# Performance work log

Measured on AMD Instinct MI355X. Metric: run time of the kernel, lower is better.

The kernel has to match this reference:

```python
import jax, jax.numpy as jnp
import numpy as np

B, S, NB, D, H = 4, 512, 32, 512, 8

def setup_inputs() -> dict:
    key = jax.random.key(0)
    ks = jax.random.split(key, 8)
    sc = 1.0 / np.sqrt(D)
    return {
        "query": jax.random.normal(ks[0], (B, S, NB, D), dtype=jnp.float32),
        "key": jax.random.normal(ks[1], (B, S, NB, D), dtype=jnp.float32),
        "value": jax.random.normal(ks[2], (B, S, NB, D), dtype=jnp.float32),
        "padding_mask": jnp.zeros((B, S, NB), dtype=jnp.float32),
        "wq": jax.random.normal(ks[3], (D, D), dtype=jnp.float32) * sc,
        "bq": jnp.zeros((D,), dtype=jnp.float32),
        "wk": jax.random.normal(ks[4], (D, D), dtype=jnp.float32) * sc,
        "bk": jnp.zeros((D,), dtype=jnp.float32),
        "wv": jax.random.normal(ks[5], (D, D), dtype=jnp.float32) * sc,
        "bv": jnp.zeros((D,), dtype=jnp.float32),
        "nhead": H,
    }

def reference(query, key, value, padding_mask, wq, bq, wk, bk, wv, bv, nhead):
    b, s, nb, d = query.shape
    dh = d // nhead
    # Linear projections (torch Linear: x @ W.T + b)
    Q = query @ wq.T + bq
    K = key @ wk.T + bk
    V = value @ wv.T + bv
    # [B, S, Nb, H, dh] -> [B, H, S, Nb, dh]
    def split_heads(x):
        return x.reshape(b, s, nb, nhead, dh).transpose(0, 3, 1, 2, 4)
    Qh, Kh, Vh = split_heads(Q), split_heads(K), split_heads(V)
    # attention over the block axis per (batch, head, seq position)
    logits = jnp.einsum('bhsnd,bhsmd->bhsnm', Qh, Kh) / jnp.sqrt(jnp.float32(dh))
    # additive mask [B, S, Nb] -> [B, 1, S, 1, Nb]
    logits = logits + padding_mask[:, None, :, None, :]
    attn_weight = jax.nn.softmax(logits, axis=-1)  # [B,H,S,Nb,Nb]
    attn_output = jnp.einsum('bhsnm,bhsmd->bhsnd', attn_weight, Vh)
    # [B,H,S,Nb,dh] -> [B,S,Nb,H,dh] -> [B,S,Nb,D]
    attn_output = attn_output.transpose(0, 2, 3, 1, 4).reshape(b, s, nb, d)
    return (attn_output, attn_weight)
```

## Files before the change

kernel.cpp:

```cpp
#include <hip/hip_runtime.h>
#include <hip/hip_bf16.h>


#define NBD (32 * 512)
#define XS_STRIDE 516

typedef __bf16 bf16x8 __attribute__((ext_vector_type(8)));
typedef float f32x16 __attribute__((ext_vector_type(16)));

__device__ __forceinline__ unsigned f2b(float f) {
  union { float f; unsigned u; } v;
  v.f = f;
  return (v.u + 0x7fffu + ((v.u >> 16) & 1u)) >> 16;
}

__device__ __forceinline__ f32x16 mfma32(uint4 a, uint4 b, f32x16 c) {
  union { uint4 u; bf16x8 v; } ua, ub;
  ua.u = a;
  ub.u = b;
  return __builtin_amdgcn_mfma_f32_32x32x16_bf16(ua.v, ub.v, c, 0, 0, 0);
}

__device__ __forceinline__ uint4 ld_lds_64x2(const unsigned short* p, unsigned byteoff) {
  const char* c = (const char*)p;
  uint2 lo = *(const uint2*)(c + byteoff);
  uint2 hi = *(const uint2*)(c + byteoff + 8);
  uint4 r;
  r.x = lo.x; r.y = lo.y; r.z = hi.x; r.w = hi.y;
  return r;
}

__device__ __forceinline__ uint4 frag_cd(const unsigned* CP, int qb, int half) {
  const unsigned s0 = __shfl_xor(CP[qb + 0], 32);
  const unsigned s1 = __shfl_xor(CP[qb + 1], 32);
  const unsigned s2 = __shfl_xor(CP[qb + 2], 32);
  const unsigned s3 = __shfl_xor(CP[qb + 3], 32);
  uint4 f;
  f.x = half ? s2 : CP[qb + 0];
  f.y = half ? s3 : CP[qb + 1];
  f.z = half ? CP[qb + 2] : s0;
  f.w = half ? CP[qb + 3] : s1;
  return f;
}

__global__ void wconv_kernel(const float* __restrict__ wq,
                             const float* __restrict__ wk,
                             const float* __restrict__ wv,
                             uint4* __restrict__ out) {
  const int g = blockIdx.x * blockDim.x + threadIdx.x;
  const int m = g >> 15;
  const int j = g & 32767;
  const int l31 = j & 31;
  const int half = (j >> 5) & 1;
  const int k = (j >> 6) & 31;
  const int tile = j >> 11;
  const float* src = (m == 0) ? wq : (m == 1) ? wk : wv;
  const float4* p = (const float4*)(src + (size_t)(tile * 32 + l31) * 512 + k * 16 + half * 8);
  float4 f0 = p[0], f1 = p[1];
  uint4 o;
  o.x = f2b(f0.x) | (f2b(f0.y) << 16);
  o.y = f2b(f0.z) | (f2b(f0.w) << 16);
  o.z = f2b(f1.x) | (f2b(f1.y) << 16);
  o.w = f2b(f1.z) | (f2b(f1.w) << 16);
  out[g] = o;
}

__global__ __launch_bounds__(512, 4)
void mhba_kernel(const float* __restrict__ q_in, const float* __restrict__ k_in,
                 const float* __restrict__ v_in, const float* __restrict__ mask,
                 const float* __restrict__ bq, const float* __restrict__ bk,
                 const float* __restrict__ bv,
                 const uint4* __restrict__ wpk,
                 float* __restrict__ out_attn,
                 float* __restrict__ out_w) {
  __shared__ unsigned short Xs[32 * XS_STRIDE];
  __shared__ __align__(16) char SCR[8][4352];

  const int bs = blockIdx.x;
  const int tid = threadIdx.x;
  const int lane = tid & 63;
  const int h = tid >> 6;
  const int l31 = lane & 31;
  const int half = lane >> 5;

  const float* srcG[3] = {k_in, q_in, v_in};
  char* scr = &SCR[h][0];

  unsigned QT[2][8], VP[2][8];

#pragma unroll
  for (int m = 0; m < 3; ++m) {
    __syncthreads();
    const float4* src4 = (const float4*)(srcG[m] + (size_t)bs * NBD);
#pragma unroll
    for (int i = 0; i < 8; ++i) {
      const int idx4 = i * 512 + tid;
      float4 f = src4[idx4];
      const int n = idx4 >> 7;
      const int k4 = idx4 & 127;
      uint2 u;
      u.x = f2b(f.x) | (f2b(f.y) << 16);
      u.y = f2b(f.z) | (f2b(f.w) << 16);
      *(uint2*)((char*)Xs + (n * (XS_STRIDE * 2) + k4 * 8)) = u;
    }
    __syncthreads();

    const int wsel = (m == 0) ? 1 : (m == 1) ? 0 : 2;
    const uint4* w0 = wpk + wsel * 32768 + (2 * h) * 2048 + half * 32 + l31;
    const uint4* w1 = w0 + 2048;
    const unsigned abase = (unsigned)(l31 * (XS_STRIDE * 2) + half * 16);

    f32x16 acc0, acc1;
#pragma unroll
    for (int r = 0; r < 16; ++r) { acc0[r] = 0.0f; acc1[r] = 0.0f; }
#pragma unroll 8
    for (int k = 0; k < 32; ++k) {
      uint4 a = ld_lds_64x2(Xs, abase + (unsigned)k * 32);
      uint4 b0 = w0[k * 64];
      uint4 b1 = w1[k * 64];
      if (m == 1) {
        acc0 = mfma32(b0, a, acc0);
        acc1 = mfma32(b1, a, acc1);
      } else {
        acc0 = mfma32(a, b0, acc0);
        acc1 = mfma32(a, b1, acc1);
      }
    }

    if (m == 0) {
      const float bc0 = bk[h * 64 + l31];
      const float bc1 = bk[h * 64 + 32 + l31];
#pragma unroll
      for (int r = 0; r < 16; ++r) {
        const int n = (r & 3) + 8 * (r >> 2) + 4 * half;
        const unsigned base = (unsigned)(n * 128);
        const unsigned sw = (unsigned)(n & 7) << 4;
        *(unsigned short*)(scr + ((base + l31 * 2) ^ sw)) =
            (unsigned short)f2b(acc0[r] + bc0);
        *(unsigned short*)(scr + ((base + 64 + l31 * 2) ^ sw)) =
            (unsigned short)f2b(acc1[r] + bc1);
      }
    } else if (m == 1) {
#pragma unroll
      for (int q = 0; q < 8; ++q) {
        const int n0 = ((2 * q) & 3) + 8 * (q >> 1) + 4 * half;
        float2 bv0 = *(const float2*)(bq + h * 64 + n0);
        float2 bv1 = *(const float2*)(bq + h * 64 + 32 + n0);
        QT[0][q] = f2b(acc0[2 * q] + bv0.x) | (f2b(acc0[2 * q + 1] + bv0.y) << 16);
        QT[1][q] = f2b(acc1[2 * q] + bv1.x) | (f2b(acc1[2 * q + 1] + bv1.y) << 16);
      }
    } else {
      const float bc0 = bv[h * 64 + l31];
      const float bc1 = bv[h * 64 + 32 + l31];
#pragma unroll
      for (int q = 0; q < 8; ++q) {
        VP[0][q] = f2b(acc0[2 * q] + bc0) | (f2b(acc0[2 * q + 1] + bc0) << 16);
        VP[1][q] = f2b(acc1[2 * q] + bc1) | (f2b(acc1[2 * q + 1] + bc1) << 16);
      }
    }
  }

  f32x16 lg;
#pragma unroll
  for (int r = 0; r < 16; ++r) lg[r] = 0.0f;
#pragma unroll
  for (int kk = 0; kk < 4; ++kk) {
    const unsigned off =
        (unsigned)(l31 * 128 + kk * 32 + half * 16) ^ ((unsigned)(l31 & 7) << 4);
    uint4 ka = *(const uint4*)(scr + off);
    uint4 qf = frag_cd(QT[kk >> 1], (kk & 1) * 4, half);
    lg = mfma32(ka, qf, lg);
  }

  const float* mrow = mask + (size_t)bs * 32;
  float w[16];
#pragma unroll
  for (int q = 0; q < 8; ++q) {
    const int mm0 = ((2 * q) & 3) + 8 * (q >> 1) + 4 * half;
    float2 mk = *(const float2*)(mrow + mm0);
    w[2 * q] = lg[2 * q] * 0.125f + mk.x;
    w[2 * q + 1] = lg[2 * q + 1] * 0.125f + mk.y;
  }
  float mx = w[0];
#pragma unroll
  for (int r = 1; r < 16; ++r) mx = fmaxf(mx, w[r]);
  mx = fmaxf(mx, __shfl_xor(mx, 32));
  float ss = 0.0f;
#pragma unroll
  for (int r = 0; r < 16; ++r) {
    w[r] = __expf(w[r] - mx);
    ss += w[r];
  }
  ss += __shfl_xor(ss, 32);
  const float inv = __frcp_rn(ss);
#pragma unroll
  for (int r = 0; r < 16; ++r) w[r] *= inv;

  unsigned PP[8];
#pragma unroll
  for (int q = 0; q < 8; ++q)
    PP[q] = f2b(w[2 * q]) | (f2b(w[2 * q + 1]) << 16);

  float* scrF = (float*)scr;
#pragma unroll
  for (int r = 0; r < 16; ++r) {
    const int mm = (r & 3) + 8 * (r >> 2) + 4 * half;
    scrF[l31 * 33 + mm] = w[r];
  }
  const int b = bs >> 9;
  const int s = bs & 511;
  float* wout = out_w + ((size_t)((b * 8 + h) * 512 + s)) * 1024;
#pragma unroll
  for (int j = 0; j < 16; ++j) {
    const int n = 2 * j + half;
    wout[n * 32 + l31] = scrF[n * 33 + l31];
  }

  f32x16 o0, o1;
#pragma unroll
  for (int r = 0; r < 16; ++r) { o0[r] = 0.0f; o1[r] = 0.0f; }
#pragma unroll
  for (int kk = 0; kk < 2; ++kk) {
    uint4 pa = frag_cd(PP, 4 * kk, half);
    uint4 vb0 = frag_cd(VP[0], 4 * kk, half);
    uint4 vb1 = frag_cd(VP[1], 4 * kk, half);
    o0 = mfma32(pa, vb0, o0);
    o1 = mfma32(pa, vb1, o1);
  }

  float* obase = out_attn + (size_t)bs * NBD + h * 64 + l31;
#pragma unroll
  for (int r = 0; r < 16; ++r) {
    const int n = (r & 3) + 8 * (r >> 2) + 4 * half;
    obase[n * 512] = o0[r];
    obase[n * 512 + 32] = o1[r];
  }
}

extern "C" void kernel_launch(void* const* d_in, const int* in_sizes, int n_in,
                              void* d_out, int out_size, void* d_ws, size_t ws_size,
                              hipStream_t stream) {
  const float* q    = (const float*)d_in[0];
  const float* k    = (const float*)d_in[1];
  const float* v    = (const float*)d_in[2];
  const float* mask = (const float*)d_in[3];
  const float* wq   = (const float*)d_in[4];
  const float* bq   = (const float*)d_in[5];
  const float* wk   = (const float*)d_in[6];
  const float* bk   = (const float*)d_in[7];
  const float* wv   = (const float*)d_in[8];
  const float* bv   = (const float*)d_in[9];

  uint4* wpk = (uint4*)d_ws;
  float* out_attn = (float*)d_out;
  float* out_w = out_attn + (size_t)4 * 512 * 32 * 512;

  wconv_kernel<<<384, 256, 0, stream>>>(wq, wk, wv, wpk);
  mhba_kernel<<<2048, 512, 0, stream>>>(q, k, v, mask, bq, bk, bv, wpk,
                                        out_attn, out_w);
}
```

Before: 234.8 us.

## Process two sequence positions per block to reuse weight fragments

```diff
diff --git a/kernel.cpp b/kernel.cpp
--- a/kernel.cpp
+++ b/kernel.cpp
@@ -4,6 +4,7 @@
 
 #define NBD (32 * 512)
 #define XS_STRIDE 516
+#define XS_BYTES (32 * XS_STRIDE * 2)
 
 typedef __bf16 bf16x8 __attribute__((ext_vector_type(8)));
 typedef float f32x16 __attribute__((ext_vector_type(16)));
@@ -73,10 +74,9 @@
                  const uint4* __restrict__ wpk,
                  float* __restrict__ out_attn,
                  float* __restrict__ out_w) {
-  __shared__ unsigned short Xs[32 * XS_STRIDE];
-  __shared__ __align__(16) char SCR[8][4352];
-
-  const int bs = blockIdx.x;
+  __shared__ unsigned short Xs[2 * 32 * XS_STRIDE];
+
+  const int bs0 = blockIdx.x * 2;
   const int tid = threadIdx.x;
   const int lane = tid & 63;
   const int h = tid >> 6;
@@ -84,156 +84,187 @@
   const int half = lane >> 5;
 
   const float* srcG[3] = {k_in, q_in, v_in};
-  char* scr = &SCR[h][0];
-
-  unsigned QT[2][8], VP[2][8];
+
+  unsigned KT[2][2][8], QT[2][2][8], VPk[2][2][8];
+
+  const unsigned abase = (unsigned)(l31 * (XS_STRIDE * 2) + half * 16);
 
 #pragma unroll
   for (int m = 0; m < 3; ++m) {
     __syncthreads();
-    const float4* src4 = (const float4*)(srcG[m] + (size_t)bs * NBD);
-#pragma unroll
-    for (int i = 0; i < 8; ++i) {
-      const int idx4 = i * 512 + tid;
-      float4 f = src4[idx4];
-      const int n = idx4 >> 7;
-      const int k4 = idx4 & 127;
-      uint2 u;
-      u.x = f2b(f.x) | (f2b(f.y) << 16);
-      u.y = f2b(f.z) | (f2b(f.w) << 16);
-      *(uint2*)((char*)Xs + (n * (XS_STRIDE * 2) + k4 * 8)) = u;
+#pragma unroll
+    for (int j = 0; j < 2; ++j) {
+      const float4* s4 = (const float4*)(srcG[m] + (size_t)(bs0 + j) * NBD);
+#pragma unroll
+      for (int i = 0; i < 8; ++i) {
+        const int idx4 = i * 512 + tid;
+        float4 f = s4[idx4];
+        const int n = idx4 >> 7;
+        const int k4 = idx4 & 127;
+        uint2 u;
+        u.x = f2b(f.x) | (f2b(f.y) << 16);
+        u.y = f2b(f.z) | (f2b(f.w) << 16);
+        *(uint2*)((char*)Xs + (j * XS_BYTES + n * (XS_STRIDE * 2) + k4 * 8)) = u;
+      }
     }
     __syncthreads();
 
     const int wsel = (m == 0) ? 1 : (m == 1) ? 0 : 2;
-    const uint4* w0 = wpk + wsel * 32768 + (2 * h) * 2048 + half * 32 + l31;
-    const uint4* w1 = w0 + 2048;
-    const unsigned abase = (unsigned)(l31 * (XS_STRIDE * 2) + half * 16);
-
-    f32x16 acc0, acc1;
-#pragma unroll
-    for (int r = 0; r < 16; ++r) { acc0[r] = 0.0f; acc1[r] = 0.0f; }
+#pragma unroll
+    for (int t = 0; t < 2; ++t) {
+      const uint4* wld = wpk + wsel * 32768 + (2 * h + t) * 2048 + half * 32 + l31;
+      f32x16 acc0, acc1;
+#pragma unroll
+      for (int r = 0; r < 16; ++r) { acc0[r] = 0.0f; acc1[r] = 0.0f; }
 #pragma unroll 8
-    for (int k = 0; k < 32; ++k) {
-      uint4 a = ld_lds_64x2(Xs, abase + (unsigned)k * 32);
-      uint4 b0 = w0[k * 64];
-      uint4 b1 = w1[k * 64];
-      if (m == 1) {
-        acc0 = mfma32(b0, a, acc0);
-        acc1 = mfma32(b1, a, acc1);
+      for (int k = 0; k < 32; ++k) {
+        uint4 b = wld[k * 64];
+        uint4 a0 = ld_lds_64x2(Xs, abase + (unsigned)k * 32);
+        uint4 a1 = ld_lds_64x2(Xs, XS_BYTES + abase + (unsigned)k * 32);
+        if (m <= 1) {
+          acc0 = mfma32(b, a0, acc0);
+          acc1 = mfma32(b, a1, acc1);
+        } else {
+          acc0 = mfma32(a0, b, acc0);
+          acc1 = mfma32(a1, b, acc1);
+        }
+      }
+      if (m == 0) {
+#pragma unroll
+        for (int q = 0; q < 8; ++q) {
+          const int n0 = ((2 * q) & 3) + 8 * (q >> 1) + 4 * half;
+          float2 bb = *(const float2*)(bk + h * 64 + t * 32 + n0);
+          KT[0][t][q] = f2b(acc0[2 * q] + bb.x) | (f2b(acc0[2 * q + 1] + bb.y) << 16);
+          KT[1][t][q] = f2b(acc1[2 * q] + bb.x) | (f2b(acc1[2 * q + 1] + bb.y) << 16);
+        }
+      } else if (m == 1) {
+#pragma unroll
+        for (int q = 0; q < 8; ++q) {
+          const int n0 = ((2 * q) & 3) + 8 * (q >> 1) + 4 * half;
+          float2 bb = *(const float2*)(bq + h * 64 + t * 32 + n0);
+          QT[0][t][q] = f2b(acc0[2 * q] + bb.x) | (f2b(acc0[2 * q + 1] + bb.y) << 16);
+          QT[1][t][q] = f2b(acc1[2 * q] + bb.x) | (f2b(acc1[2 * q + 1] + bb.y) << 16);
+        }
       } else {
-        acc0 = mfma32(a, b0, acc0);
-        acc1 = mfma32(a, b1, acc1);
-      }
-    }
-
-    if (m == 0) {
-      const float bc0 = bk[h * 64 + l31];
-      const float bc1 = bk[h * 64 + 32 + l31];
-#pragma unroll
-      for (int r = 0; r < 16; ++r) {
-        const int n = (r & 3) + 8 * (r >> 2) + 4 * half;
-        const unsigned base = (unsigned)(n * 128);
-        const unsigned sw = (unsigned)(n & 7) << 4;
-        *(unsigned short*)(scr + ((base + l31 * 2) ^ sw)) =
-            (unsigned short)f2b(acc0[r] + bc0);
-        *(unsigned short*)(scr + ((base + 64 + l31 * 2) ^ sw)) =
-            (unsigned short)f2b(acc1[r] + bc1);
-      }
-    } else if (m == 1) {
+        const float bc = bv[h * 64 + t * 32 + l31];
+#pragma unroll
+        for (int q = 0; q < 8; ++q) {
+          VPk[0][t][q] = f2b(acc0[2 * q] + bc) | (f2b(acc0[2 * q + 1] + bc) << 16);
+          VPk[1][t][q] = f2b(acc1[2 * q] + bc) | (f2b(acc1[2 * q + 1] + bc) << 16);
+        }
+      }
+    }
+  }
+
+  __syncthreads();
+#pragma unroll
+  for (int j = 0; j < 2; ++j) {
+    char* vb = (char*)Xs + h * 8192 + j * 4096;
+#pragma unroll
+    for (int t = 0; t < 2; ++t)
 #pragma unroll
       for (int q = 0; q < 8; ++q) {
         const int n0 = ((2 * q) & 3) + 8 * (q >> 1) + 4 * half;
-        float2 bv0 = *(const float2*)(bq + h * 64 + n0);
-        float2 bv1 = *(const float2*)(bq + h * 64 + 32 + n0);
-        QT[0][q] = f2b(acc0[2 * q] + bv0.x) | (f2b(acc0[2 * q + 1] + bv0.y) << 16);
-        QT[1][q] = f2b(acc1[2 * q] + bv1.x) | (f2b(acc1[2 * q + 1] + bv1.y) << 16);
-      }
-    } else {
-      const float bc0 = bv[h * 64 + l31];
-      const float bc1 = bv[h * 64 + 32 + l31];
-#pragma unroll
-      for (int q = 0; q < 8; ++q) {
-        VP[0][q] = f2b(acc0[2 * q] + bc0) | (f2b(acc0[2 * q + 1] + bc0) << 16);
-        VP[1][q] = f2b(acc1[2 * q] + bc1) | (f2b(acc1[2 * q + 1] + bc1) << 16);
-      }
-    }
+        const unsigned col = (unsigned)((t * 32 + l31) * 2);
+        const unsigned pv = VPk[j][t][q];
+        *(unsigned short*)(vb + ((n0 * 128 + col) ^ ((unsigned)(n0 & 7) << 4))) =
+            (unsigned short)(pv & 0xffff);
+        *(unsigned short*)(vb + (((n0 + 1) * 128 + col) ^ ((unsigned)((n0 + 1) & 7) << 4))) =
+            (unsigned short)(pv >> 16);
+      }
   }
 
-  f32x16 lg;
-#pragma unroll
-  for (int r = 0; r < 16; ++r) lg[r] = 0.0f;
-#pragma unroll
-  for (int kk = 0; kk < 4; ++kk) {
-    const unsigned off =
-        (unsigned)(l31 * 128 + kk * 32 + half * 16) ^ ((unsigned)(l31 & 7) << 4);
-    uint4 ka = *(const uint4*)(scr + off);
-    uint4 qf = frag_cd(QT[kk >> 1], (kk & 1) * 4, half);
-    lg = mfma32(ka, qf, lg);
-  }
-
-  const float* mrow = mask + (size_t)bs * 32;
-  float w[16];
-#pragma unroll
-  for (int q = 0; q < 8; ++q) {
-    const int mm0 = ((2 * q) & 3) + 8 * (q >> 1) + 4 * half;
-    float2 mk = *(const float2*)(mrow + mm0);
-    w[2 * q] = lg[2 * q] * 0.125f + mk.x;
-    w[2 * q + 1] = lg[2 * q + 1] * 0.125f + mk.y;
-  }
-  float mx = w[0];
-#pragma unroll
-  for (int r = 1; r < 16; ++r) mx = fmaxf(mx, w[r]);
-  mx = fmaxf(mx, __shfl_xor(mx, 32));
-  float ss = 0.0f;
-#pragma unroll
-  for (int r = 0; r < 16; ++r) {
-    w[r] = __expf(w[r] - mx);
-    ss += w[r];
-  }
-  ss += __shfl_xor(ss, 32);
-  const float inv = __frcp_rn(ss);
-#pragma unroll
-  for (int r = 0; r < 16; ++r) w[r] *= inv;
-
-  unsigned PP[8];
-#pragma unroll
-  for (int q = 0; q < 8; ++q)
-    PP[q] = f2b(w[2 * q]) | (f2b(w[2 * q + 1]) << 16);
-
-  float* scrF = (float*)scr;
-#pragma unroll
-  for (int r = 0; r < 16; ++r) {
-    const int mm = (r & 3) + 8 * (r >> 2) + 4 * half;
-    scrF[l31 * 33 + mm] = w[r];
-  }
-  const int b = bs >> 9;
-  const int s = bs & 511;
-  float* wout = out_w + ((size_t)((b * 8 + h) * 512 + s)) * 1024;
-#pragma unroll
-  for (int j = 0; j < 16; ++j) {
-    const int n = 2 * j + half;
-    wout[n * 32 + l31] = scrF[n * 33 + l31];
-  }
-
-  f32x16 o0, o1;
-#pragma unroll
-  for (int r = 0; r < 16; ++r) { o0[r] = 0.0f; o1[r] = 0.0f; }
-#pragma unroll
-  for (int kk = 0; kk < 2; ++kk) {
-    uint4 pa = frag_cd(PP, 4 * kk, half);
-    uint4 vb0 = frag_cd(VP[0], 4 * kk, half);
-    uint4 vb1 = frag_cd(VP[1], 4 * kk, half);
-    o0 = mfma32(pa, vb0, o0);
-    o1 = mfma32(pa, vb1, o1);
-  }
-
-  float* obase = out_attn + (size_t)bs * NBD + h * 64 + l31;
-#pragma unroll
-  for (int r = 0; r < 16; ++r) {
-    const int n = (r & 3) + 8 * (r >> 2) + 4 * half;
-    obase[n * 512] = o0[r];
-    obase[n * 512 + 32] = o1[r];
+#pragma unroll
+  for (int j = 0; j < 2; ++j) {
+    const int bsj = bs0 + j;
+
+    f32x16 lg;
+#pragma unroll
+    for (int r = 0; r < 16; ++r) lg[r] = 0.0f;
+#pragma unroll
+    for (int kk = 0; kk < 4; ++kk) {
+      uint4 ka = frag_cd(KT[j][kk >> 1], (kk & 1) * 4, half);
+      uint4 qf = frag_cd(QT[j][kk >> 1], (kk & 1) * 4, half);
+      lg = mfma32(ka, qf, lg);
+    }
+
+    const float* mrow = mask + (size_t)bsj * 32;
+    float w[16];
+#pragma unroll
+    for (int q = 0; q < 8; ++q) {
+      const int mm0 = ((2 * q) & 3) + 8 * (q >> 1) + 4 * half;
+      float2 mk = *(const float2*)(mrow + mm0);
+      w[2 * q] = lg[2 * q] * 0.125f + mk.x;
+      w[2 * q + 1] = lg[2 * q + 1] * 0.125f + mk.y;
+    }
+    float mx = w[0];
+#pragma unroll
+    for (int r = 1; r < 16; ++r) mx = fmaxf(mx, w[r]);
+    mx = fmaxf(mx, __shfl_xor(mx, 32));
+    float ss = 0.0f;
+#pragma unroll
+    for (int r = 0; r < 16; ++r) {
+      w[r] = __expf(w[r] - mx);
+      ss += w[r];
+    }
+    ss += __shfl_xor(ss, 32);
+    const float inv = __frcp_rn(ss);
+#pragma unroll
+    for (int r = 0; r < 16; ++r) w[r] *= inv;
+
+    unsigned PP[8];
+#pragma unroll
+    for (int q = 0; q < 8; ++q)
+      PP[q] = f2b(w[2 * q]) | (f2b(w[2 * q + 1]) << 16);
+
+    const char* vb = (const char*)Xs + h * 8192 + j * 4096;
+    f32x16 o0, o1;
+#pragma unroll
+    for (int r = 0; r < 16; ++r) { o0[r] = 0.0f; o1[r] = 0.0f; }
+#pragma unroll
+    for (int kk = 0; kk < 2; ++kk) {
+      uint4 pa = frag_cd(PP, 4 * kk, half);
+      unsigned pk0[4] = {0, 0, 0, 0}, pk1[4] = {0, 0, 0, 0};
+#pragma unroll
+      for (int jj = 0; jj < 8; ++jj) {
+        const int mr = kk * 16 + half * 8 + jj;
+        const unsigned sw = (unsigned)(mr & 7) << 4;
+        const unsigned v0 = *(const unsigned short*)(vb + ((mr * 128 + l31 * 2) ^ sw));
+        const unsigned v1 = *(const unsigned short*)(vb + ((mr * 128 + 64 + l31 * 2) ^ sw));
+        pk0[jj >> 1] |= v0 << ((jj & 1) * 16);
+        pk1[jj >> 1] |= v1 << ((jj & 1) * 16);
+      }
+      uint4 b0, b1;
+      b0.x = pk0[0]; b0.y = pk0[1]; b0.z = pk0[2]; b0.w = pk0[3];
+      b1.x = pk1[0]; b1.y = pk1[1]; b1.z = pk1[2]; b1.w = pk1[3];
+      o0 = mfma32(pa, b0, o0);
+      o1 = mfma32(pa, b1, o1);
+    }
+
+    asm volatile("" ::: "memory");
+    char* sc = (char*)Xs + h * 8192 + j * 4096;
+#pragma unroll
+    for (int r = 0; r < 16; ++r) {
+      const int mm = (r & 3) + 8 * (r >> 2) + 4 * half;
+      *(float*)(sc + ((l31 * 128 + mm * 4) ^ ((unsigned)(l31 & 7) << 4))) = w[r];
+    }
+    const int b = bsj >> 9;
+    const int s = bsj & 511;
+    float* wout = out_w + ((size_t)((b * 8 + h) * 512 + s)) * 1024;
+#pragma unroll
+    for (int jj = 0; jj < 16; ++jj) {
+      const int n = 2 * jj + half;
+      wout[n * 32 + l31] =
+          *(const float*)(sc + ((n * 128 + l31 * 4) ^ ((unsigned)(n & 7) << 4)));
+    }
+
+    float* obase = out_attn + (size_t)bsj * NBD + h * 64 + l31;
+#pragma unroll
+    for (int r = 0; r < 16; ++r) {
+      const int n = (r & 3) + 8 * (r >> 2) + 4 * half;
+      obase[n * 512] = o0[r];
+      obase[n * 512 + 32] = o1[r];
+    }
   }
 }
 
@@ -256,6 +287,6 @@
   float* out_w = out_attn + (size_t)4 * 512 * 32 * 512;
 
   wconv_kernel<<<384, 256, 0, stream>>>(wq, wk, wv, wpk);
-  mhba_kernel<<<2048, 512, 0, stream>>>(q, k, v, mask, bq, bk, bv, wpk,
+  mhba_kernel<<<1024, 512, 0, stream>>>(q, k, v, mask, bq, bk, bv, wpk,
                                         out_attn, out_w);
 }
```

New measurement: 630.4 us. +168.5%, slower.

## Process two positions per block with double-buffered LDS and prefetched global loads

Applied to the files above, without the earlier changes.

```diff
diff --git a/kernel.cpp b/kernel.cpp
--- a/kernel.cpp
+++ b/kernel.cpp
@@ -4,6 +4,7 @@
 
 #define NBD (32 * 512)
 #define XS_STRIDE 516
+#define XS_BYTES (32 * XS_STRIDE * 2)
 
 typedef __bf16 bf16x8 __attribute__((ext_vector_type(8)));
 typedef float f32x16 __attribute__((ext_vector_type(16)));
@@ -65,7 +66,7 @@
   out[g] = o;
 }
 
-__global__ __launch_bounds__(512, 4)
+__global__ __launch_bounds__(512, 2)
 void mhba_kernel(const float* __restrict__ q_in, const float* __restrict__ k_in,
                  const float* __restrict__ v_in, const float* __restrict__ mask,
                  const float* __restrict__ bq, const float* __restrict__ bk,
@@ -73,168 +74,182 @@
                  const uint4* __restrict__ wpk,
                  float* __restrict__ out_attn,
                  float* __restrict__ out_w) {
-  __shared__ unsigned short Xs[32 * XS_STRIDE];
-  __shared__ __align__(16) char SCR[8][4352];
-
-  const int bs = blockIdx.x;
+  __shared__ unsigned short Xs[2 * 2 * 32 * XS_STRIDE];
+
+  const int bs0 = blockIdx.x * 2;
   const int tid = threadIdx.x;
   const int lane = tid & 63;
   const int h = tid >> 6;
   const int l31 = lane & 31;
   const int half = lane >> 5;
 
-  const float* srcG[3] = {k_in, q_in, v_in};
-  char* scr = &SCR[h][0];
-
-  unsigned QT[2][8], VP[2][8];
-
-#pragma unroll
-  for (int m = 0; m < 3; ++m) {
-    __syncthreads();
-    const float4* src4 = (const float4*)(srcG[m] + (size_t)bs * NBD);
-#pragma unroll
-    for (int i = 0; i < 8; ++i) {
-      const int idx4 = i * 512 + tid;
-      float4 f = src4[idx4];
-      const int n = idx4 >> 7;
-      const int k4 = idx4 & 127;
-      uint2 u;
-      u.x = f2b(f.x) | (f2b(f.y) << 16);
-      u.y = f2b(f.z) | (f2b(f.w) << 16);
-      *(uint2*)((char*)Xs + (n * (XS_STRIDE * 2) + k4 * 8)) = u;
-    }
-    __syncthreads();
-
-    const int wsel = (m == 0) ? 1 : (m == 1) ? 0 : 2;
-    const uint4* w0 = wpk + wsel * 32768 + (2 * h) * 2048 + half * 32 + l31;
-    const uint4* w1 = w0 + 2048;
-    const unsigned abase = (unsigned)(l31 * (XS_STRIDE * 2) + half * 16);
-
-    f32x16 acc0, acc1;
-#pragma unroll
-    for (int r = 0; r < 16; ++r) { acc0[r] = 0.0f; acc1[r] = 0.0f; }
-#pragma unroll 8
-    for (int k = 0; k < 32; ++k) {
-      uint4 a = ld_lds_64x2(Xs, abase + (unsigned)k * 32);
-      uint4 b0 = w0[k * 64];
-      uint4 b1 = w1[k * 64];
-      if (m == 1) {
-        acc0 = mfma32(b0, a, acc0);
-        acc1 = mfma32(b1, a, acc1);
-      } else {
-        acc0 = mfma32(a, b0, acc0);
-        acc1 = mfma32(a, b1, acc1);
-      }
-    }
-
-    if (m == 0) {
-      const float bc0 = bk[h * 64 + l31];
-      const float bc1 = bk[h * 64 + 32 + l31];
-#pragma unroll
-      for (int r = 0; r < 16; ++r) {
-        const int n = (r & 3) + 8 * (r >> 2) + 4 * half;
-        const unsigned base = (unsigned)(n * 128);
-        const unsigned sw = (unsigned)(n & 7) << 4;
-        *(unsigned short*)(scr + ((base + l31 * 2) ^ sw)) =
-            (unsigned short)f2b(acc0[r] + bc0);
-        *(unsigned short*)(scr + ((base + 64 + l31 * 2) ^ sw)) =
-            (unsigned short)f2b(acc1[r] + bc1);
-      }
-    } else if (m == 1) {
-#pragma unroll
-      for (int q = 0; q < 8; ++q) {
-        const int n0 = ((2 * q) & 3) + 8 * (q >> 1) + 4 * half;
-        float2 bv0 = *(const float2*)(bq + h * 64 + n0);
-        float2 bv1 = *(const float2*)(bq + h * 64 + 32 + n0);
-        QT[0][q] = f2b(acc0[2 * q] + bv0.x) | (f2b(acc0[2 * q + 1] + bv0.y) << 16);
-        QT[1][q] = f2b(acc1[2 * q] + bv1.x) | (f2b(acc1[2 * q + 1] + bv1.y) << 16);
-      }
-    } else {
-      const float bc0 = bv[h * 64 + l31];
-      const float bc1 = bv[h * 64 + 32 + l31];
-#pragma unroll
-      for (int q = 0; q < 8; ++q) {
-        VP[0][q] = f2b(acc0[2 * q] + bc0) | (f2b(acc0[2 * q + 1] + bc0) << 16);
-        VP[1][q] = f2b(acc1[2 * q] + bc1) | (f2b(acc1[2 * q + 1] + bc1) << 16);
-      }
-    }
-  }
-
-  f32x16 lg;
-#pragma unroll
-  for (int r = 0; r < 16; ++r) lg[r] = 0.0f;
-#pragma unroll
-  for (int kk = 0; kk < 4; ++kk) {
-    const unsigned off =
-        (unsigned)(l31 * 128 + kk * 32 + half * 16) ^ ((unsigned)(l31 & 7) << 4);
-    uint4 ka = *(const uint4*)(scr + off);
-    uint4 qf = frag_cd(QT[kk >> 1], (kk & 1) * 4, half);
-    lg = mfma32(ka, qf, lg);
-  }
-
-  const float* mrow = mask + (size_t)bs * 32;
-  float w[16];
-#pragma unroll
-  for (int q = 0; q < 8; ++q) {
-    const int mm0 = ((2 * q) & 3) + 8 * (q >> 1) + 4 * half;
-    float2 mk = *(const float2*)(mrow + mm0);
-    w[2 * q] = lg[2 * q] * 0.125f + mk.x;
-    w[2 * q + 1] = lg[2 * q + 1] * 0.125f + mk.y;
-  }
-  float mx = w[0];
-#pragma unroll
-  for (int r = 1; r < 16; ++r) mx = fmaxf(mx, w[r]);
-  mx = fmaxf(mx, __shfl_xor(mx, 32));
-  float ss = 0.0f;
-#pragma unroll
-  for (int r = 0; r < 16; ++r) {
-    w[r] = __expf(w[r] - mx);
-    ss += w[r];
-  }
-  ss += __shfl_xor(ss, 32);
-  const float inv = __frcp_rn(ss);
-#pragma unroll
-  for (int r = 0; r < 16; ++r) w[r] *= inv;
-
-  unsigned PP[8];
-#pragma unroll
-  for (int q = 0; q < 8; ++q)
-    PP[q] = f2b(w[2 * q]) | (f2b(w[2 * q + 1]) << 16);
-
-  float* scrF = (float*)scr;
-#pragma unroll
-  for (int r = 0; r < 16; ++r) {
-    const int mm = (r & 3) + 8 * (r >> 2) + 4 * half;
-    scrF[l31 * 33 + mm] = w[r];
-  }
-  const int b = bs >> 9;
-  const int s = bs & 511;
-  float* wout = out_w + ((size_t)((b * 8 + h) * 512 + s)) * 1024;
-#pragma unroll
-  for (int j = 0; j < 16; ++j) {
-    const int n = 2 * j + half;
-    wout[n * 32 + l31] = scrF[n * 33 + l31];
-  }
-
-  f32x16 o0, o1;
-#pragma unroll
-  for (int r = 0; r < 16; ++r) { o0[r] = 0.0f; o1[r] = 0.0f; }
-#pragma unroll
-  for (int kk = 0; kk < 2; ++kk) {
-    uint4 pa = frag_cd(PP, 4 * kk, half);
-    uint4 vb0 = frag_cd(VP[0], 4 * kk, half);
-    uint4 vb1 = frag_cd(VP[1], 4 * kk, half);
-    o0 = mfma32(pa, vb0, o0);
-    o1 = mfma32(pa, vb1, o1);
-  }
-
-  float* obase = out_attn + (size_t)bs * NBD + h * 64 + l31;
-#pragma unroll
-  for (int r = 0; r < 16; ++r) {
-    const int n = (r & 3) + 8 * (r >> 2) + 4 * half;
-    obase[n * 512] = o0[r];
-    obase[n * 512 + 32] = o1[r];
-  }
+  unsigned short* bufA = Xs;
+  unsigned short* bufB = Xs + 2 * 32 * XS_STRIDE;
+
+  unsigned KT[2][2][8], QT[2][2][8], VP[2][2][8];
+  const unsigned abase = (unsigned)(l31 * (XS_STRIDE * 2) + half * 16);
+
+  float4 st[16];
+
+#define LOADS(SRC)                                                        \
+  {                                                                       \
+    _Pragma("unroll") for (int j = 0; j < 2; ++j) {                       \
+      const float4* s4 = (const float4*)((SRC) + (size_t)(bs0 + j) * NBD);\
+      _Pragma("unroll") for (int i = 0; i < 8; ++i)                       \
+        st[j * 8 + i] = s4[i * 512 + tid];                                \
+    }                                                                     \
+  }
+
+#define WRITE(BUF)                                                        \
+  {                                                                       \
+    _Pragma("unroll") for (int j = 0; j < 2; ++j) {                       \
+      _Pragma("unroll") for (int i = 0; i < 8; ++i) {                     \
+        const int idx4 = i * 512 + tid;                                   \
+        const int n = idx4 >> 7;                                          \
+        const int k4 = idx4 & 127;                                        \
+        float4 f = st[j * 8 + i];                                         \
+        uint2 u;                                                          \
+        u.x = f2b(f.x) | (f2b(f.y) << 16);                                \
+        u.y = f2b(f.z) | (f2b(f.w) << 16);                                \
+        *(uint2*)((char*)(BUF) + (j * XS_BYTES + n * (XS_STRIDE * 2) + k4 * 8)) = u; \
+      }                                                                   \
+    }                                                                     \
+  }
+
+#define COMPUTE(MM, BUF, WSEL, BIAS, DST, TRANSPOSED)                     \
+  {                                                                       \
+    _Pragma("unroll") for (int t = 0; t < 2; ++t) {                       \
+      const uint4* wld = wpk + (WSEL)*32768 + (2 * h + t) * 2048 + half * 32 + l31; \
+      f32x16 acc0, acc1;                                                  \
+      _Pragma("unroll") for (int r = 0; r < 16; ++r) { acc0[r] = 0.0f; acc1[r] = 0.0f; } \
+      _Pragma("unroll 8") for (int k = 0; k < 32; ++k) {                  \
+        uint4 b = wld[k * 64];                                            \
+        uint4 a0 = ld_lds_64x2((BUF), abase + (unsigned)k * 32);          \
+        uint4 a1 = ld_lds_64x2((BUF), XS_BYTES + abase + (unsigned)k * 32);\
+        if (TRANSPOSED) {                                                 \
+          acc0 = mfma32(b, a0, acc0);                                     \
+          acc1 = mfma32(b, a1, acc1);                                     \
+        } else {                                                          \
+          acc0 = mfma32(a0, b, acc0);                                     \
+          acc1 = mfma32(a1, b, acc1);                                     \
+        }                                                                 \
+      }                                                                   \
+      if (TRANSPOSED) {                                                   \
+        _Pragma("unroll") for (int q = 0; q < 8; ++q) {                   \
+          const int n0 = ((2 * q) & 3) + 8 * (q >> 1) + 4 * half;         \
+          float2 bb = *(const float2*)((BIAS) + h * 64 + t * 32 + n0);    \
+          DST[0][t][q] = f2b(acc0[2 * q] + bb.x) | (f2b(acc0[2 * q + 1] + bb.y) << 16); \
+          DST[1][t][q] = f2b(acc1[2 * q] + bb.x) | (f2b(acc1[2 * q + 1] + bb.y) << 16); \
+        }                                                                 \
+      } else {                                                            \
+        const float bc = (BIAS)[h * 64 + t * 32 + l31];                   \
+        _Pragma("unroll") for (int q = 0; q < 8; ++q) {                   \
+          DST[0][t][q] = f2b(acc0[2 * q] + bc) | (f2b(acc0[2 * q + 1] + bc) << 16); \
+          DST[1][t][q] = f2b(acc1[2 * q] + bc) | (f2b(acc1[2 * q + 1] + bc) << 16); \
+        }                                                                 \
+      }                                                                   \
+    }                                                                     \
+  }
+
+  LOADS(k_in);
+  WRITE(bufA);
+  __syncthreads();
+
+  LOADS(q_in);
+  COMPUTE(0, bufA, 1, bk, KT, 1);
+  WRITE(bufB);
+  __syncthreads();
+
+  LOADS(v_in);
+  COMPUTE(1, bufB, 0, bq, QT, 1);
+  WRITE(bufA);
+  __syncthreads();
+
+  COMPUTE(2, bufA, 2, bv, VP, 0);
+
+  asm volatile("" ::: "memory");
+  float* scrF = (float*)((char*)bufB + h * 8256);
+
+#pragma unroll
+  for (int j = 0; j < 2; ++j) {
+    const int bsj = bs0 + j;
+
+    f32x16 lg;
+#pragma unroll
+    for (int r = 0; r < 16; ++r) lg[r] = 0.0f;
+#pragma unroll
+    for (int kk = 0; kk < 4; ++kk) {
+      uint4 ka = frag_cd(KT[j][kk >> 1], (kk & 1) * 4, half);
+      uint4 qf = frag_cd(QT[j][kk >> 1], (kk & 1) * 4, half);
+      lg = mfma32(ka, qf, lg);
+    }
+
+    const float* mrow = mask + (size_t)bsj * 32;
+    float w[16];
+#pragma unroll
+    for (int q = 0; q < 8; ++q) {
+      const int mm0 = ((2 * q) & 3) + 8 * (q >> 1) + 4 * half;
+      float2 mk = *(const float2*)(mrow + mm0);
+      w[2 * q] = lg[2 * q] * 0.125f + mk.x;
+      w[2 * q + 1] = lg[2 * q + 1] * 0.125f + mk.y;
+    }
+    float mx = w[0];
+#pragma unroll
+    for (int r = 1; r < 16; ++r) mx = fmaxf(mx, w[r]);
+    mx = fmaxf(mx, __shfl_xor(mx, 32));
+    float ss = 0.0f;
+#pragma unroll
+    for (int r = 0; r < 16; ++r) {
+      w[r] = __expf(w[r] - mx);
+      ss += w[r];
+    }
+    ss += __shfl_xor(ss, 32);
+    const float inv = __frcp_rn(ss);
+#pragma unroll
+    for (int r = 0; r < 16; ++r) w[r] *= inv;
+
+    unsigned PP[8];
+#pragma unroll
+    for (int q = 0; q < 8; ++q)
+      PP[q] = f2b(w[2 * q]) | (f2b(w[2 * q + 1]) << 16);
+
+#pragma unroll
+    for (int r = 0; r < 16; ++r) {
+      const int mm = (r & 3) + 8 * (r >> 2) + 4 * half;
+      scrF[l31 * 33 + mm] = w[r];
+    }
+    const int b = bsj >> 9;
+    const int s = bsj & 511;
+    float* wout = out_w + ((size_t)((b * 8 + h) * 512 + s)) * 1024;
+#pragma unroll
+    for (int jj = 0; jj < 16; ++jj) {
+      const int n = 2 * jj + half;
+      wout[n * 32 + l31] = scrF[n * 33 + l31];
+    }
+
+    f32x16 o0, o1;
+#pragma unroll
+    for (int r = 0; r < 16; ++r) { o0[r] = 0.0f; o1[r] = 0.0f; }
+#pragma unroll
+    for (int kk = 0; kk < 2; ++kk) {
+      uint4 pa = frag_cd(PP, 4 * kk, half);
+      uint4 vb0 = frag_cd(VP[j][0], 4 * kk, half);
+      uint4 vb1 = frag_cd(VP[j][1], 4 * kk, half);
+      o0 = mfma32(pa, vb0, o0);
+      o1 = mfma32(pa, vb1, o1);
+    }
+
+    float* obase = out_attn + (size_t)bsj * NBD + h * 64 + l31;
+#pragma unroll
+    for (int r = 0; r < 16; ++r) {
+      const int n = (r & 3) + 8 * (r >> 2) + 4 * half;
+      obase[n * 512] = o0[r];
+      obase[n * 512 + 32] = o1[r];
+    }
+  }
+#undef LOADS
+#undef WRITE
+#undef COMPUTE
 }
 
 extern "C" void kernel_launch(void* const* d_in, const int* in_sizes, int n_in,
@@ -256,6 +271,6 @@
   float* out_w = out_attn + (size_t)4 * 512 * 32 * 512;
 
   wconv_kernel<<<384, 256, 0, stream>>>(wq, wk, wv, wpk);
-  mhba_kernel<<<2048, 512, 0, stream>>>(q, k, v, mask, bq, bk, bv, wpk,
+  mhba_kernel<<<1024, 512, 0, stream>>>(q, k, v, mask, bq, bk, bv, wpk,
                                         out_attn, out_w);
 }
```

After: 350.3 us. 49.2% more time.

## Double-buffer half-tile input staging to overlap global loads with MFMA

Applied to the files above, without the earlier changes.

```diff
diff --git a/kernel.cpp b/kernel.cpp
--- a/kernel.cpp
+++ b/kernel.cpp
@@ -3,7 +3,8 @@
 
 
 #define NBD (32 * 512)
-#define XS_STRIDE 516
+#define XH_STRIDE 260
+#define XH_BYTES (32 * XH_STRIDE * 2)
 
 typedef __bf16 bf16x8 __attribute__((ext_vector_type(8)));
 typedef float f32x16 __attribute__((ext_vector_type(16)));
@@ -73,7 +74,7 @@
                  const uint4* __restrict__ wpk,
                  float* __restrict__ out_attn,
                  float* __restrict__ out_w) {
-  __shared__ unsigned short Xs[32 * XS_STRIDE];
+  __shared__ unsigned short Xs[2][32 * XH_STRIDE];
   __shared__ __align__(16) char SCR[8][4352];
 
   const int bs = blockIdx.x;
@@ -83,93 +84,141 @@
   const int l31 = lane & 31;
   const int half = lane >> 5;
 
-  const float* srcG[3] = {k_in, q_in, v_in};
   char* scr = &SCR[h][0];
+  const float* srcs[3] = {k_in, q_in, v_in};
 
   unsigned QT[2][8], VP[2][8];
-
-#pragma unroll
-  for (int m = 0; m < 3; ++m) {
-    __syncthreads();
-    const float4* src4 = (const float4*)(srcG[m] + (size_t)bs * NBD);
-#pragma unroll
-    for (int i = 0; i < 8; ++i) {
-      const int idx4 = i * 512 + tid;
-      float4 f = src4[idx4];
-      const int n = idx4 >> 7;
-      const int k4 = idx4 & 127;
-      uint2 u;
-      u.x = f2b(f.x) | (f2b(f.y) << 16);
-      u.y = f2b(f.z) | (f2b(f.w) << 16);
-      *(uint2*)((char*)Xs + (n * (XS_STRIDE * 2) + k4 * 8)) = u;
+  const unsigned abase = (unsigned)(l31 * (XH_STRIDE * 2) + half * 16);
+
+  float4 st[4];
+
+#define STAGE_LOAD(M, H1)                                                  \
+  {                                                                        \
+    const float4* s4 = (const float4*)(srcs[M] + (size_t)bs * NBD);        \
+    _Pragma("unroll") for (int i = 0; i < 4; ++i) {                        \
+      const int idx4 = i * 512 + tid;                                      \
+      st[i] = s4[(idx4 >> 6) * 128 + (H1)*64 + (idx4 & 63)];               \
+    }                                                                      \
+  }
+
+#define STAGE_WRITE(P)                                                     \
+  {                                                                        \
+    _Pragma("unroll") for (int i = 0; i < 4; ++i) {                        \
+      const int idx4 = i * 512 + tid;                                      \
+      const int n = idx4 >> 6, k4 = idx4 & 63;                             \
+      uint2 u;                                                             \
+      u.x = f2b(st[i].x) | (f2b(st[i].y) << 16);                           \
+      u.y = f2b(st[i].z) | (f2b(st[i].w) << 16);                           \
+      *(uint2*)((char*)Xs[P] + (n * (XH_STRIDE * 2) + k4 * 8)) = u;        \
+    }                                                                      \
+  }
+
+#define COMPUTE_HALF(P, WSEL, H1, TRANSPOSED)                              \
+  {                                                                        \
+    const uint4* w0 = wpk + (WSEL)*32768 + (2 * h) * 2048 + (H1)*1024 +    \
+                      half * 32 + l31;                                     \
+    const uint4* w1 = w0 + 2048;                                           \
+    _Pragma("unroll 8") for (int k = 0; k < 16; ++k) {                     \
+      uint4 a = ld_lds_64x2(Xs[P], abase + (unsigned)k * 32);              \
+      uint4 b0 = w0[k * 64];                                               \
+      uint4 b1 = w1[k * 64];                                               \
+      if (TRANSPOSED) {                                                    \
+        acc0 = mfma32(b0, a, acc0);                                        \
+        acc1 = mfma32(b1, a, acc1);                                        \
+      } else {                                                             \
+        acc0 = mfma32(a, b0, acc0);                                        \
+        acc1 = mfma32(a, b1, acc1);                                        \
+      }                                                                    \
+    }                                                                      \
+  }
+
+  f32x16 acc0, acc1;
+#pragma unroll
+  for (int r = 0; r < 16; ++r) { acc0[r] = 0.0f; acc1[r] = 0.0f; }
+
+  STAGE_LOAD(0, 0);
+  STAGE_WRITE(0);
+  __syncthreads();
+
+  STAGE_LOAD(0, 1);
+  COMPUTE_HALF(0, 1, 0, 0);
+  STAGE_WRITE(1);
+  __syncthreads();
+
+  STAGE_LOAD(1, 0);
+  COMPUTE_HALF(1, 1, 1, 0);
+  {
+    const float bc0 = bk[h * 64 + l31];
+    const float bc1 = bk[h * 64 + 32 + l31];
+#pragma unroll
+    for (int r = 0; r < 16; ++r) {
+      const int n = (r & 3) + 8 * (r >> 2) + 4 * half;
+      const unsigned base = (unsigned)(n * 128);
+      const unsigned sw = (unsigned)(n & 7) << 4;
+      *(unsigned short*)(scr + ((base + l31 * 2) ^ sw)) =
+          (unsigned short)f2b(acc0[r] + bc0);
+      *(unsigned short*)(scr + ((base + 64 + l31 * 2) ^ sw)) =
+          (unsigned short)f2b(acc1[r] + bc1);
+      acc0[r] = 0.0f;
+      acc1[r] = 0.0f;
     }
-    __syncthreads();
-
-    const int wsel = (m == 0) ? 1 : (m == 1) ? 0 : 2;
-    const uint4* w0 = wpk + wsel * 32768 + (2 * h) * 2048 + half * 32 + l31;
-    const uint4* w1 = w0 + 2048;
-    const unsigned abase = (unsigned)(l31 * (XS_STRIDE * 2) + half * 16);
-
-    f32x16 acc0, acc1;
-#pragma unroll
-    for (int r = 0; r < 16; ++r) { acc0[r] = 0.0f; acc1[r] = 0.0f; }
-#pragma unroll 8
-    for (int k = 0; k < 32; ++k) {
-      uint4 a = ld_lds_64x2(Xs, abase + (unsigned)k * 32);
-      uint4 b0 = w0[k * 64];
-      uint4 b1 = w1[k * 64];
-      if (m == 1) {
-        acc0 = mfma32(b0, a, acc0);
-        acc1 = mfma32(b1, a, acc1);
-      } else {
-        acc0 = mfma32(a, b0, acc0);
-        acc1 = mfma32(a, b1, acc1);
-      }
+  }
+  STAGE_WRITE(0);
+  __syncthreads();
+
+  STAGE_LOAD(1, 1);
+  COMPUTE_HALF(0, 0, 0, 1);
+  STAGE_WRITE(1);
+  __syncthreads();
+
+  STAGE_LOAD(2, 0);
+  COMPUTE_HALF(1, 0, 1, 1);
+  {
+#pragma unroll
+    for (int q = 0; q < 8; ++q) {
+      const int n0 = ((2 * q) & 3) + 8 * (q >> 1) + 4 * half;
+      float2 bv0 = *(const float2*)(bq + h * 64 + n0);
+      float2 bv1 = *(const float2*)(bq + h * 64 + 32 + n0);
+      QT[0][q] = f2b(acc0[2 * q] + bv0.x) | (f2b(acc0[2 * q + 1] + bv0.y) << 16);
+      QT[1][q] = f2b(acc1[2 * q] + bv1.x) | (f2b(acc1[2 * q + 1] + bv1.y) << 16);
+      acc0[2 * q] = 0.0f; acc0[2 * q + 1] = 0.0f;
+      acc1[2 * q] = 0.0f; acc1[2 * q + 1] = 0.0f;
     }
-
-    if (m == 0) {
-      const float bc0 = bk[h * 64 + l31];
-      const float bc1 = bk[h * 64 + 32 + l31];
-#pragma unroll
-      for (int r = 0; r < 16; ++r) {
-        const int n = (r & 3) + 8 * (r >> 2) + 4 * half;
-        const unsigned base = (unsigned)(n * 128);
-        const unsigned sw = (unsigned)(n & 7) << 4;
-        *(unsigned short*)(scr + ((base + l31 * 2) ^ sw)) =
-            (unsigned short)f2b(acc0[r] + bc0);
-        *(unsigned short*)(scr + ((base + 64 + l31 * 2) ^ sw)) =
-            (unsigned short)f2b(acc1[r] + bc1);
-      }
-    } else if (m == 1) {
-#pragma unroll
-      for (int q = 0; q < 8; ++q) {
-        const int n0 = ((2 * q) & 3) + 8 * (q >> 1) + 4 * half;
-        float2 bv0 = *(const float2*)(bq + h * 64 + n0);
-        float2 bv1 = *(const float2*)(bq + h * 64 + 32 + n0);
-        QT[0][q] = f2b(acc0[2 * q] + bv0.x) | (f2b(acc0[2 * q + 1] + bv0.y) << 16);
-        QT[1][q] = f2b(acc1[2 * q] + bv1.x) | (f2b(acc1[2 * q + 1] + bv1.y) << 16);
-      }
-    } else {
-      const float bc0 = bv[h * 64 + l31];
-      const float bc1 = bv[h * 64 + 32 + l31];
-#pragma unroll
-      for (int q = 0; q < 8; ++q) {
-        VP[0][q] = f2b(acc0[2 * q] + bc0) | (f2b(acc0[2 * q + 1] + bc0) << 16);
-        VP[1][q] = f2b(acc1[2 * q] + bc1) | (f2b(acc1[2 * q + 1] + bc1) << 16);
-      }
+  }
+  STAGE_WRITE(0);
+  __syncthreads();
+
+  STAGE_LOAD(2, 1);
+  COMPUTE_HALF(0, 2, 0, 0);
+  STAGE_WRITE(1);
+  __syncthreads();
+
+  COMPUTE_HALF(1, 2, 1, 0);
+  {
+    const float bc0 = bv[h * 64 + l31];
+    const float bc1 = bv[h * 64 + 32 + l31];
+#pragma unroll
+    for (int q = 0; q < 8; ++q) {
+      VP[0][q] = f2b(acc0[2 * q] + bc0) | (f2b(acc0[2 * q + 1] + bc0) << 16);
+      VP[1][q] = f2b(acc1[2 * q] + bc1) | (f2b(acc1[2 * q + 1] + bc1) << 16);
     }
   }
 
-  f32x16 lg;
-#pragma unroll
-  for (int r = 0; r < 16; ++r) lg[r] = 0.0f;
+  uint4 KA[4];
 #pragma unroll
   for (int kk = 0; kk < 4; ++kk) {
     const unsigned off =
         (unsigned)(l31 * 128 + kk * 32 + half * 16) ^ ((unsigned)(l31 & 7) << 4);
-    uint4 ka = *(const uint4*)(scr + off);
+    KA[kk] = *(const uint4*)(scr + off);
+  }
+
+  f32x16 lg;
+#pragma unroll
+  for (int r = 0; r < 16; ++r) lg[r] = 0.0f;
+#pragma unroll
+  for (int kk = 0; kk < 4; ++kk) {
     uint4 qf = frag_cd(QT[kk >> 1], (kk & 1) * 4, half);
-    lg = mfma32(ka, qf, lg);
+    lg = mfma32(KA[kk], qf, lg);
   }
 
   const float* mrow = mask + (size_t)bs * 32;
@@ -201,6 +250,7 @@
   for (int q = 0; q < 8; ++q)
     PP[q] = f2b(w[2 * q]) | (f2b(w[2 * q + 1]) << 16);
 
+  asm volatile("" ::: "memory");
   float* scrF = (float*)scr;
 #pragma unroll
   for (int r = 0; r < 16; ++r) {
@@ -235,6 +285,9 @@
     obase[n * 512] = o0[r];
     obase[n * 512 + 32] = o1[r];
   }
+#undef STAGE_LOAD
+#undef STAGE_WRITE
+#undef COMPUTE_HALF
 }
 
 extern "C" void kernel_launch(void* const* d_in, const int* in_sizes, int n_in,
```

Result: slower. 245.3 us (+4.5%).
